# Optimization experiments

Measured on AMD Instinct MI355X. Metric: run time of the kernel, lower is better.

The kernel has to match this reference:

```python
import jax, jax.numpy as jnp
import numpy as np

K_HOPS = 3
ALPHA = 0.3
DELTA = 0.5
KL_EPS = 1e-10
BN_EPS = 1e-5
DEG_MIN = 1e-6

B, T, N, F_IN, H, T_OUT = 8, 12, 1536, 1, 64, 12
HID2 = 2 * H  # MLP hidden width = 128


def setup_inputs() -> dict:
    key = jax.random.key(0)
    ks = jax.random.split(key, 20)
    s = 0.05
    TH = T * H
    inp = {
        "x": jax.random.normal(ks[0], (B, T, N, F_IN), jnp.float32),
        # AdaptiveBiDiffConv weights (stored as (in, out))
        "W1": jax.random.normal(ks[1], (F_IN, H), jnp.float32) * s,
        "W2": jax.random.normal(ks[2], (F_IN, H), jnp.float32) * s,
        # encoder MLPBlock: Linear(TH,128) ReLU Linear(128,128) ReLU Linear(128,64) + proj(TH,64), BN(64)
        "enc_w1": jax.random.normal(ks[3], (TH, HID2), jnp.float32) * s,
        "enc_b1": jnp.zeros((HID2,), jnp.float32),
        "enc_w2": jax.random.normal(ks[4], (HID2, HID2), jnp.float32) * s,
        "enc_b2": jnp.zeros((HID2,), jnp.float32),
        "enc_w3": jax.random.normal(ks[5], (HID2, H), jnp.float32) * s,
        "enc_b3": jnp.zeros((H,), jnp.float32),
        "enc_proj": jax.random.normal(ks[6], (TH, H), jnp.float32) * s,
        "enc_bn_g": jnp.ones((H,), jnp.float32),
        "enc_bn_b": jnp.zeros((H,), jnp.float32),
        "enc_bn_m": jnp.zeros((H,), jnp.float32),
        "enc_bn_v": jnp.ones((H,), jnp.float32),
        # decoder MLPBlock: Linear(64,128) ReLU Linear(128,128) ReLU Linear(128,12) + proj(64,12), BN(12)
        "dec_w1": jax.random.normal(ks[7], (H, HID2), jnp.float32) * s,
        "dec_b1": jnp.zeros((HID2,), jnp.float32),
        "dec_w2": jax.random.normal(ks[8], (HID2, HID2), jnp.float32) * s,
        "dec_b2": jnp.zeros((HID2,), jnp.float32),
        "dec_w3": jax.random.normal(ks[9], (HID2, T_OUT), jnp.float32) * s,
        "dec_b3": jnp.zeros((T_OUT,), jnp.float32),
        "dec_proj": jax.random.normal(ks[10], (H, T_OUT), jnp.float32) * s,
        "dec_bn_g": jnp.ones((T_OUT,), jnp.float32),
        "dec_bn_b": jnp.zeros((T_OUT,), jnp.float32),
        "dec_bn_m": jnp.zeros((T_OUT,), jnp.float32),
        "dec_bn_v": jnp.ones((T_OUT,), jnp.float32),
    }
    return inp


def _row_norm(A):
    return A / jnp.maximum(A.sum(-1, keepdims=True), DEG_MIN)


def _mlp_block(z, w1, b1, w2, b2, w3, b3, proj, g, be, m, v):
    h = jax.nn.relu(z @ w1 + b1)
    h = jax.nn.relu(h @ w2 + b2)
    o = (h @ w3 + b3) + z @ proj
    # BatchNorm1d, eval mode over last (channel) axis
    return (o - m) / jnp.sqrt(v + BN_EPS) * g + be


def _forward(x, W1, W2,
             enc_w1, enc_b1, enc_w2, enc_b2, enc_w3, enc_b3, enc_proj,
             enc_bn_g, enc_bn_b, enc_bn_m, enc_bn_v,
             dec_w1, dec_b1, dec_w2, dec_b2, dec_w3, dec_b3, dec_proj,
             dec_bn_g, dec_bn_b, dec_bn_m, dec_bn_v):
    b, t, n, _ = x.shape
    # ---- KL adjacency (fused form: avoids (B,N,N,T) broadcast) ----
    p = jax.nn.softmax(jnp.transpose(x[..., 0], (0, 2, 1)), axis=-1)  # (B,N,T)
    logp = jnp.log(p + KL_EPS)
    # kl[b,i,j] = sum_t p_i (logp_i - logp_j)
    kl = jnp.sum(p * logp, axis=-1, keepdims=True) - jnp.einsum('bit,bjt->bij', p, logp)
    A = (kl < DELTA).astype(x.dtype)  # (B,N,N)
    A_fwd = _row_norm(A)
    A_bwd = _row_norm(jnp.swapaxes(A, -1, -2))
    # ---- bidirectional diffusion conv (x_k never updated in original loop) ----
    x_flow = x[..., :1]                    # (B,T,N,1)
    x_res = x_flow @ W1                    # (B,T,N,H)
    xw = x_flow @ W2                       # (B,T,N,H)
    fwd = jnp.einsum('bij,btjh->btih', A_fwd, xw)
    bwd = jnp.einsum('bij,btjh->btih', A_bwd, xw)
    x_p = jax.nn.relu(x_res + K_HOPS * (ALPHA * fwd + (1.0 - ALPHA) * bwd))
    # ---- temporal MLP encoder/decoder ----
    x_flat = jnp.transpose(x_p, (0, 2, 1, 3)).reshape(b, n, t * x_p.shape[-1])  # (B,N,T*H)
    x_e = _mlp_block(x_flat, enc_w1, enc_b1, enc_w2, enc_b2, enc_w3, enc_b3,
                     enc_proj, enc_bn_g, enc_bn_b, enc_bn_m, enc_bn_v)  # (B,N,H)
    x_d = _mlp_block(x_e, dec_w1, dec_b1, dec_w2, dec_b2, dec_w3, dec_b3,
                     dec_proj, dec_bn_g, dec_bn_b, dec_bn_m, dec_bn_v)  # (B,N,T_out)
    return jnp.transpose(x_d, (0, 2, 1))[..., None]  # (B,T_out,N,1)


def reference(x, W1, W2,
              enc_w1, enc_b1, enc_w2, enc_b2, enc_w3, enc_b3, enc_proj,
              enc_bn_g, enc_bn_b, enc_bn_m, enc_bn_v,
              dec_w1, dec_b1, dec_w2, dec_b2, dec_w3, dec_b3, dec_proj,
              dec_bn_g, dec_bn_b, dec_bn_m, dec_bn_v):
    return _forward(x, W1, W2,
                    enc_w1, enc_b1, enc_w2, enc_b2, enc_w3, enc_b3, enc_proj,
                    enc_bn_g, enc_bn_b, enc_bn_m, enc_bn_v,
                    dec_w1, dec_b1, dec_w2, dec_b2, dec_w3, dec_b3, dec_proj,
                    dec_bn_g, dec_bn_b, dec_bn_m, dec_bn_v)
```

## Files before the change

### kernel.cpp

```cpp
#include <hip/hip_runtime.h>
#include <hip/hip_bf16.h>


namespace {

constexpr int Bn = 8, Nn = 1536, TOUT = 12;
constexpr int Mrows = Bn * Nn;
constexpr int JS = 8;

typedef __attribute__((ext_vector_type(8))) short bf8;
typedef __attribute__((ext_vector_type(4))) float f4;
typedef unsigned short ush;

__device__ __forceinline__ float b2f(__hip_bfloat16 v) { return __bfloat162float(v); }
__device__ __forceinline__ ush f2bu(float f) {
  union { __hip_bfloat16 h; ush u; } c; c.h = __float2bfloat16(f); return c.u;
}
__device__ __forceinline__ float bu2f(ush u) {
  union { unsigned int i; float f; } c; c.i = ((unsigned)u) << 16; return c.f;
}
__device__ __forceinline__ float ldraw(const void* p, size_t i, int fl) {
  return fl ? ((const float*)p)[i] : b2f(((const __hip_bfloat16*)p)[i]);
}

__device__ __forceinline__ int detect_fl(const void* x, int tid) {
  __shared__ int cnt;
  if (tid == 0) cnt = 0;
  __syncthreads();
  const ush* u = (const ush*)x;
  int c = 0;
#pragma unroll
  for (int s = 0; s < 16; ++s) {
    ush v = u[tid + s * 256];
    if (((v >> 7) & 0xFF) >= 140) c++;
  }
  atomicAdd(&cnt, c);
  __syncthreads();
  return (cnt > 64) ? 1 : 0;
}

struct SmallTab { const void* src[16]; int n[16]; int off[16]; };
struct RepTab { const void* src[8]; int Nc[8]; int NCT[8]; int lb[9]; };

__global__ __launch_bounds__(256) void prep_all(
    const void* __restrict__ xraw, SmallTab st, RepTab rt,
    int* __restrict__ flag, float* __restrict__ CS,
    float* __restrict__ xT, float* __restrict__ sd,
    ush* __restrict__ pA, ush* __restrict__ lA,
    ush* __restrict__ phi16, ush* __restrict__ plo16,
    ush* __restrict__ lhi16, ush* __restrict__ llo16,
    ush* __restrict__ Xc, ush* __restrict__ Wf) {
  int tid = threadIdx.x;
  int fl = detect_fl(xraw, tid);
  int blk = blockIdx.x;

  if (blk < 48) {
    int row = blk * 256 + tid;
    int b = row / Nn, n = row - b * Nn;
    float xv[12];
#pragma unroll
    for (int t = 0; t < 12; ++t)
      xv[t] = ldraw(xraw, (size_t)(b * 12 + t) * Nn + n, fl);
    float mx = xv[0];
#pragma unroll
    for (int t = 1; t < 12; ++t) mx = fmaxf(mx, xv[t]);
    float e[12], Z = 0.f;
#pragma unroll
    for (int t = 0; t < 12; ++t) { e[t] = expf(xv[t] - mx); Z += e[t]; }
    float invZ = 1.f / Z;
    float sacc = 0.f;
    ush pa[32], la[32], ph[16], pl[16], lh[16], ll[16];
#pragma unroll
    for (int k = 0; k < 32; ++k) { pa[k] = 0; la[k] = 0; }
#pragma unroll
    for (int k = 0; k < 16; ++k) { ph[k] = 0; pl[k] = 0; lh[k] = 0; ll[k] = 0; }
#pragma unroll
    for (int t = 0; t < 12; ++t) {
      float pv = e[t] * invZ;
      float lv = logf(pv + 1e-10f);
      sacc += pv * lv;
      xT[(size_t)row * 12 + t] = xv[t];
      ush phv = f2bu(pv);  float plv = pv - bu2f(phv);
      ush lhv = f2bu(lv);  float llv = lv - bu2f(lhv);
      pa[t] = phv; pa[16 + t] = f2bu(plv);
      la[t] = lhv; la[16 + t] = f2bu(llv);
      ph[t] = phv; pl[t] = f2bu(plv);
      lh[t] = lhv; ll[t] = f2bu(llv);
      Xc[((size_t)(b * 16 + t)) * Nn + n] = f2bu(xv[t]);
    }
    Xc[((size_t)(b * 16 + 12)) * Nn + n] = 0x3F80;
#pragma unroll
    for (int t = 13; t < 16; ++t) Xc[((size_t)(b * 16 + t)) * Nn + n] = 0;
    sd[row] = sacc;
    {
      uint4* d = (uint4*)(pA + (size_t)row * 32);
      const uint4* s = (const uint4*)pa;
      d[0] = s[0]; d[1] = s[1]; d[2] = s[2]; d[3] = s[3];
      uint4* d2 = (uint4*)(lA + (size_t)row * 32);
      const uint4* s2 = (const uint4*)la;
      d2[0] = s2[0]; d2[1] = s2[1]; d2[2] = s2[2]; d2[3] = s2[3];
      ((uint4*)(phi16 + (size_t)row * 16))[0] = ((const uint4*)ph)[0];
      ((uint4*)(phi16 + (size_t)row * 16))[1] = ((const uint4*)ph)[1];
      ((uint4*)(plo16 + (size_t)row * 16))[0] = ((const uint4*)pl)[0];
      ((uint4*)(plo16 + (size_t)row * 16))[1] = ((const uint4*)pl)[1];
      ((uint4*)(lhi16 + (size_t)row * 16))[0] = ((const uint4*)lh)[0];
      ((uint4*)(lhi16 + (size_t)row * 16))[1] = ((const uint4*)lh)[1];
      ((uint4*)(llo16 + (size_t)row * 16))[0] = ((const uint4*)ll)[0];
      ((uint4*)(llo16 + (size_t)row * 16))[1] = ((const uint4*)ll)[1];
    }
  } else if (blk < 146) {
    int idx = (blk - 48) * 256 + tid;
    if (idx >= rt.lb[8]) return;
    int mi = 0;
#pragma unroll
    for (int i = 1; i < 8; ++i) if (idx >= rt.lb[i]) mi = i;
    int li = idx - rt.lb[mi];
    int NCT = rt.NCT[mi], Nc = rt.Nc[mi];
    int per = NCT * 64;
    int c0 = li / per, rem = li - c0 * per;
    int ct = rem >> 6, l = rem & 63;
    int q = l >> 4, m = l & 15;
    int col = ct * 16 + m;
    ush* d = Wf + (size_t)idx * 8;
#pragma unroll
    for (int j = 0; j < 8; ++j) {
      int k = c0 * 32 + q * 8 + j;
      d[j] = (col < Nc) ? f2bu(ldraw(rt.src[mi], (size_t)k * Nc + col, fl)) : 0;
    }
  } else {
    for (int i = 0; i < 16; ++i)
      for (int e = tid; e < st.n[i]; e += 256)
        CS[st.off[i] + e] = ldraw(st.src[i], e, fl);
    if (tid == 0) flag[0] = fl;
  }
}

__global__ __launch_bounds__(256) void kl_mfma(
    const ush* __restrict__ pA, const ush* __restrict__ lA,
    const ush* __restrict__ phi16, const ush* __restrict__ plo16,
    const ush* __restrict__ lhi16, const ush* __restrict__ llo16,
    const ush* __restrict__ Xc, const float* __restrict__ sd,
    float* __restrict__ psf, float* __restrict__ psb) {
  __shared__ ush T1[4][512], T2[4][512];
  int tid = threadIdx.x, w = tid >> 6, l = tid & 63, q = l >> 4, n = l & 15;
  int blk = blockIdx.x;
  int b = blk / 192, rem = blk % 192, ig = rem >> 3, js = rem & 7;
  int i0 = ig * 64 + w * 16;
  int rowb = b * Nn;

  if (q >= 2) {
    uint4 z4 = {0, 0, 0, 0};
    *(uint4*)(&T1[w][(size_t)l * 8]) = z4;
    *(uint4*)(&T2[w][(size_t)l * 8]) = z4;
  }

  bf8 z8 = {0, 0, 0, 0, 0, 0, 0, 0};
  bf8 aP = *(const bf8*)(pA + ((size_t)(rowb + i0 + n)) * 32 + q * 8);
  bf8 aL = *(const bf8*)(lA + ((size_t)(rowb + i0 + n)) * 32 + q * 8);
  bf8 aPh = (q < 2) ? aP : z8;
  bf8 aLh = (q < 2) ? aL : z8;
  float selfI[4];
#pragma unroll
  for (int r = 0; r < 4; ++r) selfI[r] = sd[rowb + i0 + q * 4 + r];

  f4 accF = {0.f, 0.f, 0.f, 0.f}, accB = {0.f, 0.f, 0.f, 0.f};

  for (int jt = 0; jt < 12; ++jt) {
    int jl = js * 192 + jt * 16;
    size_t bb = ((size_t)(rowb + jl + n)) * 16 + (q & 1) * 8;
    bf8 bLh = *(const bf8*)(lhi16 + bb);
    bf8 bLo = *(const bf8*)(llo16 + bb);
    bf8 bPh = *(const bf8*)(phi16 + bb);
    bf8 bPo = *(const bf8*)(plo16 + bb);
    float selfJ = sd[rowb + jl + n];

    f4 s1 = {0.f, 0.f, 0.f, 0.f}, s2 = {0.f, 0.f, 0.f, 0.f};
    s1 = __builtin_amdgcn_mfma_f32_16x16x32_bf16(aP, bLh, s1, 0, 0, 0);
    s1 = __builtin_amdgcn_mfma_f32_16x16x32_bf16(aPh, bLo, s1, 0, 0, 0);
    s2 = __builtin_amdgcn_mfma_f32_16x16x32_bf16(aL, bPh, s2, 0, 0, 0);
    s2 = __builtin_amdgcn_mfma_f32_16x16x32_bf16(aLh, bPo, s2, 0, 0, 0);

    int qk = n >> 3, kj = n & 7;
#pragma unroll
    for (int r = 0; r < 4; ++r) {
      int pos = (qk * 16 + q * 4 + r) * 8 + kj;
      T1[w][pos] = (selfI[r] - s1[r] < 0.5f) ? (ush)0x3F80 : (ush)0;
      T2[w][pos] = (selfJ - s2[r] < 0.5f) ? (ush)0x3F80 : (ush)0;
    }
    bf8 af1 = *(const bf8*)(&T1[w][(size_t)l * 8]);
    bf8 af2 = *(const bf8*)(&T2[w][(size_t)l * 8]);
    bf8 xfr = (q < 2)
        ? *(const bf8*)(Xc + ((size_t)(b * 16 + n)) * Nn + jl + q * 8) : z8;
    accF = __builtin_amdgcn_mfma_f32_16x16x32_bf16(af1, xfr, accF, 0, 0, 0);
    accB = __builtin_amdgcn_mfma_f32_16x16x32_bf16(af2, xfr, accB, 0, 0, 0);
  }
#pragma unroll
  for (int r = 0; r < 4; ++r) {
    size_t o = ((size_t)js * Mrows + rowb + i0 + q * 4 + r) * 16 + n;
    psf[o] = accF[r];
    psb[o] = accB[r];
  }
}

__global__ __launch_bounds__(256) void fused_mlp(
    const float* __restrict__ xT,
    const float* __restrict__ psf, const float* __restrict__ psb,
    const float* __restrict__ CS, const ush* __restrict__ Wf,
    const int* __restrict__ flag, void* __restrict__ outp) {
  __shared__ float xs[16][12], ccs[16][12];
  __shared__ float sfs[16][16], sbs[16][16];
  __shared__ float ws1[64], ws2[64];
  __shared__ ush hf[2048], hg[2048], xf[1024];
  __shared__ f4 red[4][64];

  int tid = threadIdx.x, w = tid >> 6, l = tid & 63, q = l >> 4, n = l & 15;
  int r0 = blockIdx.x * 16;

  {
    int r = tid >> 4, t = tid & 15;
    float a = 0.f, b = 0.f;
#pragma unroll
    for (int js = 0; js < JS; ++js) {
      size_t o = ((size_t)js * Mrows + r0 + r) * 16 + t;
      a += psf[o];
      b += psb[o];
    }
    sfs[r][t] = a;
    sbs[r][t] = b;
    if (tid < 128) { if (tid < 64) ws1[tid] = CS[tid]; else ws2[tid - 64] = CS[tid]; }
    if (tid < 192) {
      int rr = tid / 12, tt = tid - rr * 12;
      xs[rr][tt] = xT[(size_t)(r0 + rr) * 12 + tt];
    }
  }
  __syncthreads();
  if (tid < 192) {
    int rr = tid / 12, tt = tid - rr * 12;
    float irs = 1.f / fmaxf(sfs[rr][12], 1e-6f);
    float ics = 1.f / fmaxf(sbs[rr][12], 1e-6f);
    ccs[rr][tt] = 3.0f * (0.3f * sfs[rr][tt] * irs + 0.7f * sbs[rr][tt] * ics);
  }
  __syncthreads();

  auto zregen = [&](int c0) -> bf8 {
    int t = c0 >> 1, h0 = (c0 & 1) * 32 + q * 8;
    float xv = xs[n][t], cv = ccs[n][t];
    union { bf8 v; ush u[8]; } au;
#pragma unroll
    for (int j = 0; j < 8; ++j)
      au.u[j] = f2bu(fmaxf(fmaf(xv, ws1[h0 + j], cv * ws2[h0 + j]), 0.f));
    return au.v;
  };
  auto fpos = [&](int ct, int r) -> int {
    return ((ct >> 1) * 64 + ((ct & 1) * 2 + (n >> 3)) * 16 + q * 4 + r) * 8 + (n & 7);
  };

  {
    f4 a0 = {0.f, 0.f, 0.f, 0.f}, a1 = {0.f, 0.f, 0.f, 0.f};
    for (int c0 = 0; c0 < 24; ++c0) {
      bf8 a = zregen(c0);
      const ush* wb = Wf + ((size_t)(c0 * 8 + 2 * w) * 64 + l) * 8;
      bf8 b0 = *(const bf8*)wb;
      bf8 b1 = *(const bf8*)(wb + 512);
      a0 = __builtin_amdgcn_mfma_f32_16x16x32_bf16(a, b0, a0, 0, 0, 0);
      a1 = __builtin_amdgcn_mfma_f32_16x16x32_bf16(a, b1, a1, 0, 0, 0);
    }
#pragma unroll
    for (int u2 = 0; u2 < 2; ++u2) {
      int ct = 2 * w + u2;
      f4 acc = u2 ? a1 : a0;
      float bz = CS[128 + ct * 16 + n];
#pragma unroll
      for (int r = 0; r < 4; ++r)
        hf[fpos(ct, r)] = f2bu(fmaxf(acc[r] + bz, 0.f));
    }
  }
  __syncthreads();

  {
    f4 a0 = {0.f, 0.f, 0.f, 0.f}, a1 = {0.f, 0.f, 0.f, 0.f};
    for (int c0 = 0; c0 < 4; ++c0) {
      bf8 a = *(const bf8*)(&hf[(size_t)(c0 * 64 + l) * 8]);
      const ush* wb = Wf + 98304 + ((size_t)(c0 * 8 + 2 * w) * 64 + l) * 8;
      bf8 b0 = *(const bf8*)wb;
      bf8 b1 = *(const bf8*)(wb + 512);
      a0 = __builtin_amdgcn_mfma_f32_16x16x32_bf16(a, b0, a0, 0, 0, 0);
      a1 = __builtin_amdgcn_mfma_f32_16x16x32_bf16(a, b1, a1, 0, 0, 0);
    }
    __syncthreads();
#pragma unroll
    for (int u2 = 0; u2 < 2; ++u2) {
      int ct = 2 * w + u2;
      f4 acc = u2 ? a1 : a0;
      float bz = CS[256 + ct * 16 + n];
#pragma unroll
      for (int r = 0; r < 4; ++r)
        hg[fpos(ct, r)] = f2bu(fmaxf(acc[r] + bz, 0.f));
    }
  }
  __syncthreads();

  {
    f4 a3 = {0.f, 0.f, 0.f, 0.f};
    for (int c0 = 0; c0 < 4; ++c0) {
      bf8 a = *(const bf8*)(&hg[(size_t)(c0 * 64 + l) * 8]);
      bf8 b = *(const bf8*)(Wf + 114688 + ((size_t)(c0 * 4 + w) * 64 + l) * 8);
      a3 = __builtin_amdgcn_mfma_f32_16x16x32_bf16(a, b, a3, 0, 0, 0);
    }
    for (int c0 = 0; c0 < 24; ++c0) {
      bf8 a = zregen(c0);
      bf8 b = *(const bf8*)(Wf + 122880 + ((size_t)(c0 * 4 + w) * 64 + l) * 8);
      a3 = __builtin_amdgcn_mfma_f32_16x16x32_bf16(a, b, a3, 0, 0, 0);
    }
    int col = w * 16 + n;
    float g = CS[448 + col], be = CS[512 + col], mm = CS[576 + col], vv = CS[640 + col];
    float sc = g / sqrtf(vv + 1e-5f);
    float sh = be - mm * sc;
    float bz = CS[384 + col];
#pragma unroll
    for (int r = 0; r < 4; ++r)
      xf[fpos(w, r)] = f2bu((a3[r] + bz) * sc + sh);
  }
  __syncthreads();

  {
    f4 a0 = {0.f, 0.f, 0.f, 0.f}, a1 = {0.f, 0.f, 0.f, 0.f};
    for (int c0 = 0; c0 < 2; ++c0) {
      bf8 a = *(const bf8*)(&xf[(size_t)(c0 * 64 + l) * 8]);
      const ush* wb = Wf + 172032 + ((size_t)(c0 * 8 + 2 * w) * 64 + l) * 8;
      bf8 b0 = *(const bf8*)wb;
      bf8 b1 = *(const bf8*)(wb + 512);
      a0 = __builtin_amdgcn_mfma_f32_16x16x32_bf16(a, b0, a0, 0, 0, 0);
      a1 = __builtin_amdgcn_mfma_f32_16x16x32_bf16(a, b1, a1, 0, 0, 0);
    }
    __syncthreads();
#pragma unroll
    for (int u2 = 0; u2 < 2; ++u2) {
      int ct = 2 * w + u2;
      f4 acc = u2 ? a1 : a0;
      float bz = CS[704 + ct * 16 + n];
#pragma unroll
      for (int r = 0; r < 4; ++r)
        hf[fpos(ct, r)] = f2bu(fmaxf(acc[r] + bz, 0.f));
    }
  }
  __syncthreads();

  {
    f4 a0 = {0.f, 0.f, 0.f, 0.f}, a1 = {0.f, 0.f, 0.f, 0.f};
    for (int c0 = 0; c0 < 4; ++c0) {
      bf8 a = *(const bf8*)(&hf[(size_t)(c0 * 64 + l) * 8]);
      const ush* wb = Wf + 180224 + ((size_t)(c0 * 8 + 2 * w) * 64 + l) * 8;
      bf8 b0 = *(const bf8*)wb;
      bf8 b1 = *(const bf8*)(wb + 512);
      a0 = __builtin_amdgcn_mfma_f32_16x16x32_bf16(a, b0, a0, 0, 0, 0);
      a1 = __builtin_amdgcn_mfma_f32_16x16x32_bf16(a, b1, a1, 0, 0, 0);
    }
    __syncthreads();
#pragma unroll
    for (int u2 = 0; u2 < 2; ++u2) {
      int ct = 2 * w + u2;
      f4 acc = u2 ? a1 : a0;
      float bz = CS[832 + ct * 16 + n];
#pragma unroll
      for (int r = 0; r < 4; ++r)
        hg[fpos(ct, r)] = f2bu(fmaxf(acc[r] + bz, 0.f));
    }
  }
  __syncthreads();

  {
    f4 ao = {0.f, 0.f, 0.f, 0.f};
    {
      bf8 a = *(const bf8*)(&hg[(size_t)(w * 64 + l) * 8]);
      bf8 b = *(const bf8*)(Wf + 196608 + ((size_t)w * 64 + l) * 8);
      ao = __builtin_amdgcn_mfma_f32_16x16x32_bf16(a, b, ao, 0, 0, 0);
    }
    if (w < 2) {
      bf8 a = *(const bf8*)(&xf[(size_t)(w * 64 + l) * 8]);
      bf8 b = *(const bf8*)(Wf + 198656 + ((size_t)w * 64 + l) * 8);
      ao = __builtin_amdgcn_mfma_f32_16x16x32_bf16(a, b, ao, 0, 0, 0);
    }
    red[w][l] = ao;
  }
  __syncthreads();
  if (w == 0) {
    f4 s = red[0][l] + red[1][l] + red[2][l] + red[3][l];
    int fl = flag[0];
    if (n < 12) {
      float bz = CS[960 + n];
      float g = CS[972 + n], be = CS[984 + n], mm = CS[996 + n], vv = CS[1008 + n];
      float sc = g / sqrtf(vv + 1e-5f);
      float sh = be - mm * sc;
#pragma unroll
      for (int r = 0; r < 4; ++r) {
        int row = r0 + q * 4 + r;
        int bb = row / Nn, nn = row - bb * Nn;
        size_t oi = ((size_t)bb * TOUT + n) * Nn + nn;
        float ov = (s[r] + bz) * sc + sh;
        if (fl) ((float*)outp)[oi] = ov;
        else    ((ush*)outp)[oi] = f2bu(ov);
      }
    }
  }
}

}

extern "C" void kernel_launch(void* const* d_in, const int* in_sizes, int n_in,
                              void* d_out, int out_size, void* d_ws, size_t ws_size,
                              hipStream_t stream) {
  float* f = (float*)d_ws;
  int* flag = (int*)d_ws;
  float* CS  = f + 16;
  float* xT  = f + 1040;
  float* sd  = f + 148496;
  float* psf = f + 160784;
  float* psb = f + 1733648;
  ush* U = (ush*)(f + 3306512);
  ush* pA    = U;
  ush* lA    = U + 393216;
  ush* phi16 = U + 786432;
  ush* plo16 = U + 983040;
  ush* lhi16 = U + 1179648;
  ush* llo16 = U + 1376256;
  ush* Xc    = U + 1572864;
  ush* Wf    = U + 1769472;

  SmallTab st;
  {
    const int idxs[16] = {1, 2, 4, 6, 8, 10, 11, 12, 13, 15, 17, 19, 21, 22, 23, 24};
    const int ns[16]   = {64, 64, 128, 128, 64, 64, 64, 64, 64, 128, 128, 12, 12, 12, 12, 12};
    int off = 0;
    for (int i = 0; i < 16; ++i) {
      st.src[i] = d_in[idxs[i]]; st.n[i] = ns[i]; st.off[i] = off; off += ns[i];
    }
  }
  RepTab rt;
  {
    const int idxs[8]  = {3, 5, 7, 9, 14, 16, 18, 20};
    const int rNc[8]   = {128, 128, 64, 64, 128, 128, 12, 12};
    const int rNCT[8]  = {8, 8, 4, 4, 8, 8, 1, 1};
    const int rlb[9]   = {0, 12288, 14336, 15360, 21504, 22528, 24576, 24832, 24960};
    for (int i = 0; i < 8; ++i) {
      rt.src[i] = d_in[idxs[i]]; rt.Nc[i] = rNc[i]; rt.NCT[i] = rNCT[i];
    }
    for (int i = 0; i < 9; ++i) rt.lb[i] = rlb[i];
  }

  prep_all<<<147, 256, 0, stream>>>(d_in[0], st, rt, flag, CS, xT, sd,
                                    pA, lA, phi16, plo16, lhi16, llo16, Xc, Wf);
  kl_mfma<<<1536, 256, 0, stream>>>(pA, lA, phi16, plo16, lhi16, llo16,
                                    Xc, sd, psf, psb);
  fused_mlp<<<768, 256, 0, stream>>>(xT, psf, psb, CS, Wf, flag, d_out);
}
```

Before: 155.6 us.

## Interleave KL B-operand arrays and process two row tiles per MLP block

Packs the four separate hi/lo bf16 arrays for log-probabilities and probabilities into one interleaved 64-element-per-row buffer, so each kl_mfma lane reads a single contiguous row. The fused MLP kernel now runs 512 threads per block covering two 16-row tiles with separate shared buffers, which halves the block count and lets each block's weight loads be shared across more rows. It also drops the extra __syncthreads inside the MLP stages, which is safe because the read and write buffers alternate (hf→hg). In exchange, shared memory per block and register pressure rise, and fewer blocks are resident.

```diff
diff --git a/kernel.cpp b/kernel.cpp
--- a/kernel.cpp
+++ b/kernel.cpp
@@ -47,9 +47,7 @@
     int* __restrict__ flag, float* __restrict__ CS,
     float* __restrict__ xT, float* __restrict__ sd,
     ush* __restrict__ pA, ush* __restrict__ lA,
-    ush* __restrict__ phi16, ush* __restrict__ plo16,
-    ush* __restrict__ lhi16, ush* __restrict__ llo16,
-    ush* __restrict__ Xc, ush* __restrict__ Wf) {
+    ush* __restrict__ Pk, ush* __restrict__ Xc, ush* __restrict__ Wf) {
   int tid = threadIdx.x;
   int fl = detect_fl(xraw, tid);
   int blk = blockIdx.x;
@@ -69,11 +67,11 @@
     for (int t = 0; t < 12; ++t) { e[t] = expf(xv[t] - mx); Z += e[t]; }
     float invZ = 1.f / Z;
     float sacc = 0.f;
-    ush pa[32], la[32], ph[16], pl[16], lh[16], ll[16];
+    ush pa[32], la[32], pk[64];
 #pragma unroll
     for (int k = 0; k < 32; ++k) { pa[k] = 0; la[k] = 0; }
 #pragma unroll
-    for (int k = 0; k < 16; ++k) { ph[k] = 0; pl[k] = 0; lh[k] = 0; ll[k] = 0; }
+    for (int k = 0; k < 64; ++k) pk[k] = 0;
 #pragma unroll
     for (int t = 0; t < 12; ++t) {
       float pv = e[t] * invZ;
@@ -84,8 +82,10 @@
       ush lhv = f2bu(lv);  float llv = lv - bu2f(lhv);
       pa[t] = phv; pa[16 + t] = f2bu(plv);
       la[t] = lhv; la[16 + t] = f2bu(llv);
-      ph[t] = phv; pl[t] = f2bu(plv);
-      lh[t] = lhv; ll[t] = f2bu(llv);
+      pk[t] = lhv;
+      pk[16 + t] = f2bu(llv);
+      pk[32 + t] = phv;
+      pk[48 + t] = f2bu(plv);
       Xc[((size_t)(b * 16 + t)) * Nn + n] = f2bu(xv[t]);
     }
     Xc[((size_t)(b * 16 + 12)) * Nn + n] = 0x3F80;
@@ -99,14 +99,10 @@
       uint4* d2 = (uint4*)(lA + (size_t)row * 32);
       const uint4* s2 = (const uint4*)la;
       d2[0] = s2[0]; d2[1] = s2[1]; d2[2] = s2[2]; d2[3] = s2[3];
-      ((uint4*)(phi16 + (size_t)row * 16))[0] = ((const uint4*)ph)[0];
-      ((uint4*)(phi16 + (size_t)row * 16))[1] = ((const uint4*)ph)[1];
-      ((uint4*)(plo16 + (size_t)row * 16))[0] = ((const uint4*)pl)[0];
-      ((uint4*)(plo16 + (size_t)row * 16))[1] = ((const uint4*)pl)[1];
-      ((uint4*)(lhi16 + (size_t)row * 16))[0] = ((const uint4*)lh)[0];
-      ((uint4*)(lhi16 + (size_t)row * 16))[1] = ((const uint4*)lh)[1];
-      ((uint4*)(llo16 + (size_t)row * 16))[0] = ((const uint4*)ll)[0];
-      ((uint4*)(llo16 + (size_t)row * 16))[1] = ((const uint4*)ll)[1];
+      uint4* d3 = (uint4*)(Pk + (size_t)row * 64);
+      const uint4* s3 = (const uint4*)pk;
+#pragma unroll
+      for (int v = 0; v < 8; ++v) d3[v] = s3[v];
     }
   } else if (blk < 146) {
     int idx = (blk - 48) * 256 + tid;
@@ -137,9 +133,8 @@
 
 __global__ __launch_bounds__(256) void kl_mfma(
     const ush* __restrict__ pA, const ush* __restrict__ lA,
-    const ush* __restrict__ phi16, const ush* __restrict__ plo16,
-    const ush* __restrict__ lhi16, const ush* __restrict__ llo16,
-    const ush* __restrict__ Xc, const float* __restrict__ sd,
+    const ush* __restrict__ Pk, const ush* __restrict__ Xc,
+    const float* __restrict__ sd,
     float* __restrict__ psf, float* __restrict__ psb) {
   __shared__ ush T1[4][512], T2[4][512];
   int tid = threadIdx.x, w = tid >> 6, l = tid & 63, q = l >> 4, n = l & 15;
@@ -167,11 +162,11 @@
 
   for (int jt = 0; jt < 12; ++jt) {
     int jl = js * 192 + jt * 16;
-    size_t bb = ((size_t)(rowb + jl + n)) * 16 + (q & 1) * 8;
-    bf8 bLh = *(const bf8*)(lhi16 + bb);
-    bf8 bLo = *(const bf8*)(llo16 + bb);
-    bf8 bPh = *(const bf8*)(phi16 + bb);
-    bf8 bPo = *(const bf8*)(plo16 + bb);
+    const ush* pb = Pk + ((size_t)(rowb + jl + n)) * 64 + (q & 1) * 8;
+    bf8 bLh = *(const bf8*)(pb);
+    bf8 bLo = *(const bf8*)(pb + 16);
+    bf8 bPh = *(const bf8*)(pb + 32);
+    bf8 bPo = *(const bf8*)(pb + 48);
     float selfJ = sd[rowb + jl + n];
 
     f4 s1 = {0.f, 0.f, 0.f, 0.f}, s2 = {0.f, 0.f, 0.f, 0.f};
@@ -202,39 +197,41 @@
   }
 }
 
-__global__ __launch_bounds__(256) void fused_mlp(
+__global__ __launch_bounds__(512) void fused_mlp(
     const float* __restrict__ xT,
     const float* __restrict__ psf, const float* __restrict__ psb,
     const float* __restrict__ CS, const ush* __restrict__ Wf,
     const int* __restrict__ flag, void* __restrict__ outp) {
-  __shared__ float xs[16][12], ccs[16][12];
-  __shared__ float sfs[16][16], sbs[16][16];
+  __shared__ float xs[32][12], ccs[32][12];
+  __shared__ float sfs[32][16], sbs[32][16];
   __shared__ float ws1[64], ws2[64];
-  __shared__ ush hf[2048], hg[2048], xf[1024];
-  __shared__ f4 red[4][64];
+  __shared__ ush hf[2][2048], hg[2][2048], xf[2][1024];
+  __shared__ f4 red[2][4][64];
 
   int tid = threadIdx.x, w = tid >> 6, l = tid & 63, q = l >> 4, n = l & 15;
-  int r0 = blockIdx.x * 16;
+  int tile = w >> 2, ws_ = w & 3;
+  int r0b = blockIdx.x * 32;
+  int r0 = r0b + tile * 16;
 
   {
     int r = tid >> 4, t = tid & 15;
     float a = 0.f, b = 0.f;
 #pragma unroll
     for (int js = 0; js < JS; ++js) {
-      size_t o = ((size_t)js * Mrows + r0 + r) * 16 + t;
+      size_t o = ((size_t)js * Mrows + r0b + r) * 16 + t;
       a += psf[o];
       b += psb[o];
     }
     sfs[r][t] = a;
     sbs[r][t] = b;
     if (tid < 128) { if (tid < 64) ws1[tid] = CS[tid]; else ws2[tid - 64] = CS[tid]; }
-    if (tid < 192) {
+    if (tid < 384) {
       int rr = tid / 12, tt = tid - rr * 12;
-      xs[rr][tt] = xT[(size_t)(r0 + rr) * 12 + tt];
-    }
-  }
-  __syncthreads();
-  if (tid < 192) {
+      xs[rr][tt] = xT[(size_t)(r0b + rr) * 12 + tt];
+    }
+  }
+  __syncthreads();
+  if (tid < 384) {
     int rr = tid / 12, tt = tid - rr * 12;
     float irs = 1.f / fmaxf(sfs[rr][12], 1e-6f);
     float ics = 1.f / fmaxf(sbs[rr][12], 1e-6f);
@@ -244,7 +241,7 @@
 
   auto zregen = [&](int c0) -> bf8 {
     int t = c0 >> 1, h0 = (c0 & 1) * 32 + q * 8;
-    float xv = xs[n][t], cv = ccs[n][t];
+    float xv = xs[tile * 16 + n][t], cv = ccs[tile * 16 + n][t];
     union { bf8 v; ush u[8]; } au;
 #pragma unroll
     for (int j = 0; j < 8; ++j)
@@ -255,11 +252,15 @@
     return ((ct >> 1) * 64 + ((ct & 1) * 2 + (n >> 3)) * 16 + q * 4 + r) * 8 + (n & 7);
   };
 
+  ush* hfT = hf[tile];
+  ush* hgT = hg[tile];
+  ush* xfT = xf[tile];
+
   {
     f4 a0 = {0.f, 0.f, 0.f, 0.f}, a1 = {0.f, 0.f, 0.f, 0.f};
     for (int c0 = 0; c0 < 24; ++c0) {
       bf8 a = zregen(c0);
-      const ush* wb = Wf + ((size_t)(c0 * 8 + 2 * w) * 64 + l) * 8;
+      const ush* wb = Wf + ((size_t)(c0 * 8 + 2 * ws_) * 64 + l) * 8;
       bf8 b0 = *(const bf8*)wb;
       bf8 b1 = *(const bf8*)(wb + 512);
       a0 = __builtin_amdgcn_mfma_f32_16x16x32_bf16(a, b0, a0, 0, 0, 0);
@@ -267,12 +268,12 @@
     }
 #pragma unroll
     for (int u2 = 0; u2 < 2; ++u2) {
-      int ct = 2 * w + u2;
+      int ct = 2 * ws_ + u2;
       f4 acc = u2 ? a1 : a0;
       float bz = CS[128 + ct * 16 + n];
 #pragma unroll
       for (int r = 0; r < 4; ++r)
-        hf[fpos(ct, r)] = f2bu(fmaxf(acc[r] + bz, 0.f));
+        hfT[fpos(ct, r)] = f2bu(fmaxf(acc[r] + bz, 0.f));
     }
   }
   __syncthreads();
@@ -280,22 +281,21 @@
   {
     f4 a0 = {0.f, 0.f, 0.f, 0.f}, a1 = {0.f, 0.f, 0.f, 0.f};
     for (int c0 = 0; c0 < 4; ++c0) {
-      bf8 a = *(const bf8*)(&hf[(size_t)(c0 * 64 + l) * 8]);
-      const ush* wb = Wf + 98304 + ((size_t)(c0 * 8 + 2 * w) * 64 + l) * 8;
+      bf8 a = *(const bf8*)(&hfT[(size_t)(c0 * 64 + l) * 8]);
+      const ush* wb = Wf + 98304 + ((size_t)(c0 * 8 + 2 * ws_) * 64 + l) * 8;
       bf8 b0 = *(const bf8*)wb;
       bf8 b1 = *(const bf8*)(wb + 512);
       a0 = __builtin_amdgcn_mfma_f32_16x16x32_bf16(a, b0, a0, 0, 0, 0);
       a1 = __builtin_amdgcn_mfma_f32_16x16x32_bf16(a, b1, a1, 0, 0, 0);
     }
-    __syncthreads();
 #pragma unroll
     for (int u2 = 0; u2 < 2; ++u2) {
-      int ct = 2 * w + u2;
+      int ct = 2 * ws_ + u2;
       f4 acc = u2 ? a1 : a0;
       float bz = CS[256 + ct * 16 + n];
 #pragma unroll
       for (int r = 0; r < 4; ++r)
-        hg[fpos(ct, r)] = f2bu(fmaxf(acc[r] + bz, 0.f));
+        hgT[fpos(ct, r)] = f2bu(fmaxf(acc[r] + bz, 0.f));
     }
   }
   __syncthreads();
@@ -303,45 +303,44 @@
   {
     f4 a3 = {0.f, 0.f, 0.f, 0.f};
     for (int c0 = 0; c0 < 4; ++c0) {
-      bf8 a = *(const bf8*)(&hg[(size_t)(c0 * 64 + l) * 8]);
-      bf8 b = *(const bf8*)(Wf + 114688 + ((size_t)(c0 * 4 + w) * 64 + l) * 8);
+      bf8 a = *(const bf8*)(&hgT[(size_t)(c0 * 64 + l) * 8]);
+      bf8 b = *(const bf8*)(Wf + 114688 + ((size_t)(c0 * 4 + ws_) * 64 + l) * 8);
       a3 = __builtin_amdgcn_mfma_f32_16x16x32_bf16(a, b, a3, 0, 0, 0);
     }
     for (int c0 = 0; c0 < 24; ++c0) {
       bf8 a = zregen(c0);
-      bf8 b = *(const bf8*)(Wf + 122880 + ((size_t)(c0 * 4 + w) * 64 + l) * 8);
+      bf8 b = *(const bf8*)(Wf + 122880 + ((size_t)(c0 * 4 + ws_) * 64 + l) * 8);
       a3 = __builtin_amdgcn_mfma_f32_16x16x32_bf16(a, b, a3, 0, 0, 0);
     }
-    int col = w * 16 + n;
+    int col = ws_ * 16 + n;
     float g = CS[448 + col], be = CS[512 + col], mm = CS[576 + col], vv = CS[640 + col];
     float sc = g / sqrtf(vv + 1e-5f);
     float sh = be - mm * sc;
     float bz = CS[384 + col];
 #pragma unroll
     for (int r = 0; r < 4; ++r)
-      xf[fpos(w, r)] = f2bu((a3[r] + bz) * sc + sh);
+      xfT[fpos(ws_, r)] = f2bu((a3[r] + bz) * sc + sh);
   }
   __syncthreads();
 
   {
     f4 a0 = {0.f, 0.f, 0.f, 0.f}, a1 = {0.f, 0.f, 0.f, 0.f};
     for (int c0 = 0; c0 < 2; ++c0) {
-      bf8 a = *(const bf8*)(&xf[(size_t)(c0 * 64 + l) * 8]);
-      const ush* wb = Wf + 172032 + ((size_t)(c0 * 8 + 2 * w) * 64 + l) * 8;
+      bf8 a = *(const bf8*)(&xfT[(size_t)(c0 * 64 + l) * 8]);
+      const ush* wb = Wf + 172032 + ((size_t)(c0 * 8 + 2 * ws_) * 64 + l) * 8;
       bf8 b0 = *(const bf8*)wb;
       bf8 b1 = *(const bf8*)(wb + 512);
       a0 = __builtin_amdgcn_mfma_f32_16x16x32_bf16(a, b0, a0, 0, 0, 0);
       a1 = __builtin_amdgcn_mfma_f32_16x16x32_bf16(a, b1, a1, 0, 0, 0);
     }
-    __syncthreads();
 #pragma unroll
     for (int u2 = 0; u2 < 2; ++u2) {
-      int ct = 2 * w + u2;
+      int ct = 2 * ws_ + u2;
       f4 acc = u2 ? a1 : a0;
       float bz = CS[704 + ct * 16 + n];
 #pragma unroll
       for (int r = 0; r < 4; ++r)
-        hf[fpos(ct, r)] = f2bu(fmaxf(acc[r] + bz, 0.f));
+        hfT[fpos(ct, r)] = f2bu(fmaxf(acc[r] + bz, 0.f));
     }
   }
   __syncthreads();
@@ -349,22 +348,21 @@
   {
     f4 a0 = {0.f, 0.f, 0.f, 0.f}, a1 = {0.f, 0.f, 0.f, 0.f};
     for (int c0 = 0; c0 < 4; ++c0) {
-      bf8 a = *(const bf8*)(&hf[(size_t)(c0 * 64 + l) * 8]);
-      const ush* wb = Wf + 180224 + ((size_t)(c0 * 8 + 2 * w) * 64 + l) * 8;
+      bf8 a = *(const bf8*)(&hfT[(size_t)(c0 * 64 + l) * 8]);
+      const ush* wb = Wf + 180224 + ((size_t)(c0 * 8 + 2 * ws_) * 64 + l) * 8;
       bf8 b0 = *(const bf8*)wb;
       bf8 b1 = *(const bf8*)(wb + 512);
       a0 = __builtin_amdgcn_mfma_f32_16x16x32_bf16(a, b0, a0, 0, 0, 0);
       a1 = __builtin_amdgcn_mfma_f32_16x16x32_bf16(a, b1, a1, 0, 0, 0);
     }
-    __syncthreads();
 #pragma unroll
     for (int u2 = 0; u2 < 2; ++u2) {
-      int ct = 2 * w + u2;
+      int ct = 2 * ws_ + u2;
       f4 acc = u2 ? a1 : a0;
       float bz = CS[832 + ct * 16 + n];
 #pragma unroll
       for (int r = 0; r < 4; ++r)
-        hg[fpos(ct, r)] = f2bu(fmaxf(acc[r] + bz, 0.f));
+        hgT[fpos(ct, r)] = f2bu(fmaxf(acc[r] + bz, 0.f));
     }
   }
   __syncthreads();
@@ -372,20 +370,20 @@
   {
     f4 ao = {0.f, 0.f, 0.f, 0.f};
     {
-      bf8 a = *(const bf8*)(&hg[(size_t)(w * 64 + l) * 8]);
-      bf8 b = *(const bf8*)(Wf + 196608 + ((size_t)w * 64 + l) * 8);
+      bf8 a = *(const bf8*)(&hgT[(size_t)(ws_ * 64 + l) * 8]);
+      bf8 b = *(const bf8*)(Wf + 196608 + ((size_t)ws_ * 64 + l) * 8);
       ao = __builtin_amdgcn_mfma_f32_16x16x32_bf16(a, b, ao, 0, 0, 0);
     }
-    if (w < 2) {
-      bf8 a = *(const bf8*)(&xf[(size_t)(w * 64 + l) * 8]);
-      bf8 b = *(const bf8*)(Wf + 198656 + ((size_t)w * 64 + l) * 8);
+    if (ws_ < 2) {
+      bf8 a = *(const bf8*)(&xfT[(size_t)(ws_ * 64 + l) * 8]);
+      bf8 b = *(const bf8*)(Wf + 198656 + ((size_t)ws_ * 64 + l) * 8);
       ao = __builtin_amdgcn_mfma_f32_16x16x32_bf16(a, b, ao, 0, 0, 0);
     }
-    red[w][l] = ao;
-  }
-  __syncthreads();
-  if (w == 0) {
-    f4 s = red[0][l] + red[1][l] + red[2][l] + red[3][l];
+    red[tile][ws_][l] = ao;
+  }
+  __syncthreads();
+  if (ws_ == 0) {
+    f4 s = red[tile][0][l] + red[tile][1][l] + red[tile][2][l] + red[tile][3][l];
     int fl = flag[0];
     if (n < 12) {
       float bz = CS[960 + n];
@@ -420,10 +418,7 @@
   ush* U = (ush*)(f + 3306512);
   ush* pA    = U;
   ush* lA    = U + 393216;
-  ush* phi16 = U + 786432;
-  ush* plo16 = U + 983040;
-  ush* lhi16 = U + 1179648;
-  ush* llo16 = U + 1376256;
+  ush* Pk    = U + 786432;
   ush* Xc    = U + 1572864;
   ush* Wf    = U + 1769472;
 
@@ -449,8 +444,7 @@
   }
 
   prep_all<<<147, 256, 0, stream>>>(d_in[0], st, rt, flag, CS, xT, sd,
-                                    pA, lA, phi16, plo16, lhi16, llo16, Xc, Wf);
-  kl_mfma<<<1536, 256, 0, stream>>>(pA, lA, phi16, plo16, lhi16, llo16,
-                                    Xc, sd, psf, psb);
-  fused_mlp<<<768, 256, 0, stream>>>(xT, psf, psb, CS, Wf, flag, d_out);
-}
+                                    pA, lA, Pk, Xc, Wf);
+  kl_mfma<<<1536, 256, 0, stream>>>(pA, lA, Pk, Xc, sd, psf, psb);
+  fused_mlp<<<384, 512, 0, stream>>>(xT, psf, psb, CS, Wf, flag, d_out);
+}
```

New measurement: 178.1 us. +14.4%, slower.

## Split KL j-range finer, pack P/L halves per row, double-buffer LDS masks

Applied to the files above, without the earlier changes.

Doubles the number of j-splits in the KL threshold kernel (JS from 8 to 16, six tiles per block, 3072 blocks) to expose more parallelism. The four separate hi/lo P and L arrays are packed into one 64-element row per node, so each tile fetch touches a single contiguous region. Also double-buffers the LDS mask tiles, fully unrolls the j loop with the Xc load hoisted, and drops one barrier in the fused MLP. The cost is twice as many partial-sum buffers for the downstream MLP kernel to write and read.

```diff
diff --git a/kernel.cpp b/kernel.cpp
--- a/kernel.cpp
+++ b/kernel.cpp
@@ -6,7 +6,8 @@
 
 constexpr int Bn = 8, Nn = 1536, TOUT = 12;
 constexpr int Mrows = Bn * Nn;
-constexpr int JS = 8;
+constexpr int JS = 16;
+constexpr int JT = 6;
 
 typedef __attribute__((ext_vector_type(8))) short bf8;
 typedef __attribute__((ext_vector_type(4))) float f4;
@@ -47,9 +48,7 @@
     int* __restrict__ flag, float* __restrict__ CS,
     float* __restrict__ xT, float* __restrict__ sd,
     ush* __restrict__ pA, ush* __restrict__ lA,
-    ush* __restrict__ phi16, ush* __restrict__ plo16,
-    ush* __restrict__ lhi16, ush* __restrict__ llo16,
-    ush* __restrict__ Xc, ush* __restrict__ Wf) {
+    ush* __restrict__ Pk, ush* __restrict__ Xc, ush* __restrict__ Wf) {
   int tid = threadIdx.x;
   int fl = detect_fl(xraw, tid);
   int blk = blockIdx.x;
@@ -69,11 +68,11 @@
     for (int t = 0; t < 12; ++t) { e[t] = expf(xv[t] - mx); Z += e[t]; }
     float invZ = 1.f / Z;
     float sacc = 0.f;
-    ush pa[32], la[32], ph[16], pl[16], lh[16], ll[16];
+    ush pa[32], la[32], pk[64];
 #pragma unroll
     for (int k = 0; k < 32; ++k) { pa[k] = 0; la[k] = 0; }
 #pragma unroll
-    for (int k = 0; k < 16; ++k) { ph[k] = 0; pl[k] = 0; lh[k] = 0; ll[k] = 0; }
+    for (int k = 0; k < 64; ++k) pk[k] = 0;
 #pragma unroll
     for (int t = 0; t < 12; ++t) {
       float pv = e[t] * invZ;
@@ -84,8 +83,10 @@
       ush lhv = f2bu(lv);  float llv = lv - bu2f(lhv);
       pa[t] = phv; pa[16 + t] = f2bu(plv);
       la[t] = lhv; la[16 + t] = f2bu(llv);
-      ph[t] = phv; pl[t] = f2bu(plv);
-      lh[t] = lhv; ll[t] = f2bu(llv);
+      pk[t] = lhv;
+      pk[16 + t] = f2bu(llv);
+      pk[32 + t] = phv;
+      pk[48 + t] = f2bu(plv);
       Xc[((size_t)(b * 16 + t)) * Nn + n] = f2bu(xv[t]);
     }
     Xc[((size_t)(b * 16 + 12)) * Nn + n] = 0x3F80;
@@ -99,14 +100,10 @@
       uint4* d2 = (uint4*)(lA + (size_t)row * 32);
       const uint4* s2 = (const uint4*)la;
       d2[0] = s2[0]; d2[1] = s2[1]; d2[2] = s2[2]; d2[3] = s2[3];
-      ((uint4*)(phi16 + (size_t)row * 16))[0] = ((const uint4*)ph)[0];
-      ((uint4*)(phi16 + (size_t)row * 16))[1] = ((const uint4*)ph)[1];
-      ((uint4*)(plo16 + (size_t)row * 16))[0] = ((const uint4*)pl)[0];
-      ((uint4*)(plo16 + (size_t)row * 16))[1] = ((const uint4*)pl)[1];
-      ((uint4*)(lhi16 + (size_t)row * 16))[0] = ((const uint4*)lh)[0];
-      ((uint4*)(lhi16 + (size_t)row * 16))[1] = ((const uint4*)lh)[1];
-      ((uint4*)(llo16 + (size_t)row * 16))[0] = ((const uint4*)ll)[0];
-      ((uint4*)(llo16 + (size_t)row * 16))[1] = ((const uint4*)ll)[1];
+      uint4* d3 = (uint4*)(Pk + (size_t)row * 64);
+      const uint4* s3 = (const uint4*)pk;
+#pragma unroll
+      for (int v = 0; v < 8; ++v) d3[v] = s3[v];
     }
   } else if (blk < 146) {
     int idx = (blk - 48) * 256 + tid;
@@ -137,21 +134,22 @@
 
 __global__ __launch_bounds__(256) void kl_mfma(
     const ush* __restrict__ pA, const ush* __restrict__ lA,
-    const ush* __restrict__ phi16, const ush* __restrict__ plo16,
-    const ush* __restrict__ lhi16, const ush* __restrict__ llo16,
-    const ush* __restrict__ Xc, const float* __restrict__ sd,
+    const ush* __restrict__ Pk, const ush* __restrict__ Xc,
+    const float* __restrict__ sd,
     float* __restrict__ psf, float* __restrict__ psb) {
-  __shared__ ush T1[4][512], T2[4][512];
+  __shared__ ush T1[2][4][512], T2[2][4][512];
   int tid = threadIdx.x, w = tid >> 6, l = tid & 63, q = l >> 4, n = l & 15;
   int blk = blockIdx.x;
-  int b = blk / 192, rem = blk % 192, ig = rem >> 3, js = rem & 7;
+  int b = blk / 384, rem = blk % 384, ig = rem >> 4, js = rem & 15;
   int i0 = ig * 64 + w * 16;
   int rowb = b * Nn;
 
   if (q >= 2) {
     uint4 z4 = {0, 0, 0, 0};
-    *(uint4*)(&T1[w][(size_t)l * 8]) = z4;
-    *(uint4*)(&T2[w][(size_t)l * 8]) = z4;
+    *(uint4*)(&T1[0][w][(size_t)l * 8]) = z4;
+    *(uint4*)(&T1[1][w][(size_t)l * 8]) = z4;
+    *(uint4*)(&T2[0][w][(size_t)l * 8]) = z4;
+    *(uint4*)(&T2[1][w][(size_t)l * 8]) = z4;
   }
 
   bf8 z8 = {0, 0, 0, 0, 0, 0, 0, 0};
@@ -165,14 +163,18 @@
 
   f4 accF = {0.f, 0.f, 0.f, 0.f}, accB = {0.f, 0.f, 0.f, 0.f};
 
-  for (int jt = 0; jt < 12; ++jt) {
-    int jl = js * 192 + jt * 16;
-    size_t bb = ((size_t)(rowb + jl + n)) * 16 + (q & 1) * 8;
-    bf8 bLh = *(const bf8*)(lhi16 + bb);
-    bf8 bLo = *(const bf8*)(llo16 + bb);
-    bf8 bPh = *(const bf8*)(phi16 + bb);
-    bf8 bPo = *(const bf8*)(plo16 + bb);
+#pragma unroll
+  for (int jt = 0; jt < JT; ++jt) {
+    int jb = jt & 1;
+    int jl = js * 96 + jt * 16;
+    const ush* pb = Pk + ((size_t)(rowb + jl + n)) * 64 + (q & 1) * 8;
+    bf8 bLh = *(const bf8*)(pb);
+    bf8 bLo = *(const bf8*)(pb + 16);
+    bf8 bPh = *(const bf8*)(pb + 32);
+    bf8 bPo = *(const bf8*)(pb + 48);
     float selfJ = sd[rowb + jl + n];
+    bf8 xfr = (q < 2)
+        ? *(const bf8*)(Xc + ((size_t)(b * 16 + n)) * Nn + jl + q * 8) : z8;
 
     f4 s1 = {0.f, 0.f, 0.f, 0.f}, s2 = {0.f, 0.f, 0.f, 0.f};
     s1 = __builtin_amdgcn_mfma_f32_16x16x32_bf16(aP, bLh, s1, 0, 0, 0);
@@ -184,13 +186,11 @@
 #pragma unroll
     for (int r = 0; r < 4; ++r) {
       int pos = (qk * 16 + q * 4 + r) * 8 + kj;
-      T1[w][pos] = (selfI[r] - s1[r] < 0.5f) ? (ush)0x3F80 : (ush)0;
-      T2[w][pos] = (selfJ - s2[r] < 0.5f) ? (ush)0x3F80 : (ush)0;
-    }
-    bf8 af1 = *(const bf8*)(&T1[w][(size_t)l * 8]);
-    bf8 af2 = *(const bf8*)(&T2[w][(size_t)l * 8]);
-    bf8 xfr = (q < 2)
-        ? *(const bf8*)(Xc + ((size_t)(b * 16 + n)) * Nn + jl + q * 8) : z8;
+      T1[jb][w][pos] = (selfI[r] - s1[r] < 0.5f) ? (ush)0x3F80 : (ush)0;
+      T2[jb][w][pos] = (selfJ - s2[r] < 0.5f) ? (ush)0x3F80 : (ush)0;
+    }
+    bf8 af1 = *(const bf8*)(&T1[jb][w][(size_t)l * 8]);
+    bf8 af2 = *(const bf8*)(&T2[jb][w][(size_t)l * 8]);
     accF = __builtin_amdgcn_mfma_f32_16x16x32_bf16(af1, xfr, accF, 0, 0, 0);
     accB = __builtin_amdgcn_mfma_f32_16x16x32_bf16(af2, xfr, accB, 0, 0, 0);
   }
@@ -287,7 +287,6 @@
       a0 = __builtin_amdgcn_mfma_f32_16x16x32_bf16(a, b0, a0, 0, 0, 0);
       a1 = __builtin_amdgcn_mfma_f32_16x16x32_bf16(a, b1, a1, 0, 0, 0);
     }
-    __syncthreads();
 #pragma unroll
     for (int u2 = 0; u2 < 2; ++u2) {
       int ct = 2 * w + u2;
@@ -416,14 +415,11 @@
   float* xT  = f + 1040;
   float* sd  = f + 148496;
   float* psf = f + 160784;
-  float* psb = f + 1733648;
-  ush* U = (ush*)(f + 3306512);
+  float* psb = f + 3306512;
+  ush* U = (ush*)(f + 6452240);
   ush* pA    = U;
   ush* lA    = U + 393216;
-  ush* phi16 = U + 786432;
-  ush* plo16 = U + 983040;
-  ush* lhi16 = U + 1179648;
-  ush* llo16 = U + 1376256;
+  ush* Pk    = U + 786432;
   ush* Xc    = U + 1572864;
   ush* Wf    = U + 1769472;
 
@@ -449,8 +445,7 @@
   }
 
   prep_all<<<147, 256, 0, stream>>>(d_in[0], st, rt, flag, CS, xT, sd,
-                                    pA, lA, phi16, plo16, lhi16, llo16, Xc, Wf);
-  kl_mfma<<<1536, 256, 0, stream>>>(pA, lA, phi16, plo16, lhi16, llo16,
-                                    Xc, sd, psf, psb);
+                                    pA, lA, Pk, Xc, Wf);
+  kl_mfma<<<3072, 256, 0, stream>>>(pA, lA, Pk, Xc, sd, psf, psb);
   fused_mlp<<<768, 256, 0, stream>>>(xT, psf, psb, CS, Wf, flag, d_out);
 }
```

Result: slower. 183.9 us (+18.2%).
